# Kernel optimization log

Hardware: AMD Instinct MI355X
Metric: run time of the kernel (lower is better)

The kernel has to match this reference:

```python
import jax, jax.numpy as jnp
import numpy as np

NUM_QUANTIZERS = 8
CODEBOOK_SIZE = 1024
DIM = 256
COMMITMENT_WEIGHT = 0.25


def setup_inputs() -> dict:
    key = jax.random.key(0)
    kz, kc = jax.random.split(key)
    z = jax.random.normal(kz, (32, 1024, DIM), dtype=jnp.float32)
    # nn.init.uniform_(cb.weight, -1/codebook_size, 1/codebook_size) per quantizer
    bound = 1.0 / CODEBOOK_SIZE
    codebooks = jax.random.uniform(
        kc, (NUM_QUANTIZERS, CODEBOOK_SIZE, DIM), dtype=jnp.float32,
        minval=-bound, maxval=bound)
    return {"z": z, "codebooks": codebooks}


def reference(z, codebooks):
    """z: [B,T,D]; codebooks: [Q,K,D]. Returns (quantized, all_indices [Q,B,T], vq_loss)."""
    sg = jax.lax.stop_gradient

    def step(carry, cb):
        residual, quantized = carry
        # squared-distance matrix [B,T,K]: ||r||^2 - 2 r.cb^T + ||cb||^2
        dists = (jnp.sum(residual * residual, axis=-1, keepdims=True)
                 - 2.0 * jnp.einsum('btd,kd->btk', residual, cb)
                 + jnp.sum(cb * cb, axis=-1))
        indices = jnp.argmin(dists, axis=-1)            # [B,T]
        q = cb[indices]                                  # [B,T,D]
        codebook_loss = jnp.mean((q - sg(residual)) ** 2)
        commit_loss = jnp.mean((residual - sg(q)) ** 2)
        loss = codebook_loss + COMMITMENT_WEIGHT * commit_loss
        q_st = residual + sg(q - residual)               # straight-through
        quantized = quantized + q_st
        residual = residual - q_st
        return (residual, quantized), (indices, loss)

    init = (z, jnp.zeros_like(z))
    (_, quantized), (all_indices, losses) = jax.lax.scan(step, init, codebooks)
    vq_loss = jnp.sum(losses)
    return quantized, all_indices, vq_loss
```

## Files before the change

kernel.cpp:

```cpp
#include <hip/hip_runtime.h>

#define QN 8
#define KN 1024
#define DN 256
#define NROWS 32768
#define IDX_BASE 8388608
#define LOSS_OFF 8650752
#define MARGIN 5e-3f
#define LCAP 3072u

#define WS_LOSS 0
#define WS_CNORM 8
#define WS_CSPLIT 12623880

#define SM_RES   0
#define SM_LCAND 66560
#define SM_CHC   78848
#define SM_ANS   79360
#define SM_RMIN  79616
#define SM_LCNT  79872
#define SM_BYTES 79888
#define RESW 260

typedef __attribute__((ext_vector_type(8))) short short8v;
typedef __attribute__((ext_vector_type(4))) float f32x4;

static __device__ __forceinline__ unsigned short f2bf(float x) {
  unsigned int u = __float_as_uint(x);
  unsigned int r = (u + 0x7fffu + ((u >> 16) & 1u)) >> 16;
  return (unsigned short)r;
}

static __device__ __forceinline__ unsigned cvt_pk_bf16(float lo, float hi) {
  unsigned r;
  asm("v_cvt_pk_bf16_f32 %0, %1, %2" : "=v"(r) : "v"(lo), "v"(hi));
  return r;
}

__device__ __forceinline__ float sum256_sq_np(const float* p) {
  float h[2];
#pragma unroll
  for (int half = 0; half < 2; ++half) {
    const float* a = p + half * 128;
    float r[8];
#pragma unroll
    for (int j = 0; j < 8; ++j) r[j] = __fmul_rn(a[j], a[j]);
    for (int i = 8; i < 128; i += 8) {
#pragma unroll
      for (int j = 0; j < 8; ++j) r[j] = __fadd_rn(r[j], __fmul_rn(a[i + j], a[i + j]));
    }
    h[half] = __fadd_rn(__fadd_rn(__fadd_rn(r[0], r[1]), __fadd_rn(r[2], r[3])),
                        __fadd_rn(__fadd_rn(r[4], r[5]), __fadd_rn(r[6], r[7])));
  }
  return __fadd_rn(h[0], h[1]);
}

__global__ void rvq_prep_norm(const float* __restrict__ cb, float* __restrict__ ws) {
  int g = blockIdx.x * blockDim.x + threadIdx.x;
  if (g < 8) ws[WS_LOSS + g] = 0.f;
  if (g < QN * KN) ws[WS_CNORM + g] = sum256_sq_np(cb + (size_t)g * DN);
}

__global__ void rvq_prep_cast(const float* __restrict__ cb, unsigned short* __restrict__ cs) {
  int gid = blockIdx.x * blockDim.x + threadIdx.x;
  uint4* s4 = (uint4*)cs;
#pragma unroll
  for (int k = 0; k < 2; ++k) {
    int ci = gid + k * 131072;
    int q = ci >> 15, rem = ci & 32767;
    int lane = rem & 63, fid = rem >> 6;
    int j = fid & 1, s = (fid >> 1) & 1, kk = (fid >> 2) & 3, wc = (fid >> 4) & 3, c = fid >> 6;
    int code = wc * 32 + j * 16 + (lane & 15);
    int doff = kk * 64 + s * 32 + (lane >> 4) * 8;
    const float4* src = (const float4*)(cb + ((size_t)(q * 1024 + c * 128 + code) * 256 + doff));
    float4 v0 = src[0], v1 = src[1];
    uint4 w;
    w.x = (unsigned)f2bf(v0.x) | ((unsigned)f2bf(v0.y) << 16);
    w.y = (unsigned)f2bf(v0.z) | ((unsigned)f2bf(v0.w) << 16);
    w.z = (unsigned)f2bf(v1.x) | ((unsigned)f2bf(v1.y) << 16);
    w.w = (unsigned)f2bf(v1.z) | ((unsigned)f2bf(v1.w) << 16);
    s4[ci] = w;
  }
}

__global__ __launch_bounds__(256, 2) void rvq_fused_all(const float* __restrict__ z,
                                                        const float* __restrict__ cb,
                                                        float* __restrict__ ws,
                                                        float* __restrict__ out) {
  extern __shared__ __align__(16) char smem[];
  float* RES = (float*)(smem + SM_RES);
  unsigned int* lcand = (unsigned int*)(smem + SM_LCAND);
  unsigned long long* chc = (unsigned long long*)(smem + SM_CHC);
  float* an_s = (float*)(smem + SM_ANS);
  unsigned int* rowmin = (unsigned int*)(smem + SM_RMIN);
  unsigned int* lcnt = (unsigned int*)(smem + SM_LCNT);

  const int tid = threadIdx.x;
  const int row0 = blockIdx.x * 64;
  const int wv = tid >> 6, lane = tid & 63, quad = lane >> 4, l15 = lane & 15;
  const int wr = wv >> 1, wc = wv & 1;

  const float4* zb = (const float4*)(z + (size_t)row0 * DN);
#pragma unroll
  for (int k = 0; k < 16; ++k) {
    int fi = k * 256 + tid;
    int rr = fi >> 6, dd = (fi & 63) * 4;
    *(float4*)&RES[rr * RESW + dd] = zb[fi];
  }
  __syncthreads();
  if (tid < 64) an_s[tid] = sum256_sq_np(&RES[tid * RESW]);

  const uint4* Bf = (const uint4*)((const unsigned short*)(ws + WS_CSPLIT));

#pragma unroll 1
  for (int q = 0; q < QN; ++q) {
    const bool last = (q == QN - 1);

    __syncthreads();
    if (tid < 64) {
      rowmin[tid] = 0x7f7fffffu;
      chc[tid] = ~0ull;
    }
    if (tid == 0) *lcnt = 0u;

    short8v areg[2][2][4];
#pragma unroll
    for (int kk = 0; kk < 4; ++kk) {
#pragma unroll
      for (int s = 0; s < 2; ++s) {
#pragma unroll
        for (int i = 0; i < 2; ++i) {
          int ra = wr * 32 + i * 16 + l15;
          int g = kk * 8 + s * 4 + quad;
          const float* fp = &RES[ra * RESW + g * 8];
          float4 v0 = *(const float4*)fp;
          float4 v1 = *(const float4*)(fp + 4);
          uint4 w;
          w.x = cvt_pk_bf16(v0.x, v0.y);
          w.y = cvt_pk_bf16(v0.z, v0.w);
          w.z = cvt_pk_bf16(v1.x, v1.y);
          w.w = cvt_pk_bf16(v1.z, v1.w);
          areg[i][s][kk] = *(short8v*)&w;
        }
      }
    }
    __syncthreads();

    const uint4* Bl = Bf + ((size_t)q * 32768 + lane);
    const float* cnq_g = ws + WS_CNORM + q * KN;
    for (int c = 0; c < 8; ++c) {
      float cnr[4];
#pragma unroll
      for (int j = 0; j < 4; ++j) cnr[j] = cnq_g[c * 128 + wc * 64 + j * 16 + l15];

      f32x4 acc[2][4];
#pragma unroll
      for (int i = 0; i < 2; ++i)
#pragma unroll
        for (int j = 0; j < 4; ++j) acc[i][j] = (f32x4){0.f, 0.f, 0.f, 0.f};

      const uint4* Bc = Bl + c * 4096;
#pragma unroll
      for (int kk = 0; kk < 4; ++kk) {
        uint4 braw[2][4];
#pragma unroll
        for (int s = 0; s < 2; ++s)
#pragma unroll
          for (int j = 0; j < 4; ++j)
            braw[s][j] = Bc[(wc * 2 + (j >> 1)) * 1024 + kk * 256 + s * 128 + (j & 1) * 64];
#pragma unroll
        for (int s = 0; s < 2; ++s)
#pragma unroll
          for (int i = 0; i < 2; ++i)
#pragma unroll
            for (int j = 0; j < 4; ++j)
              acc[i][j] = __builtin_amdgcn_mfma_f32_16x16x32_bf16(
                  areg[i][s][kk], *(const short8v*)&braw[s][j], acc[i][j], 0, 0, 0);
      }

#pragma unroll
      for (int i = 0; i < 2; ++i) {
#pragma unroll
        for (int reg = 0; reg < 4; ++reg) {
          int rl = wr * 32 + i * 16 + quad * 4 + reg;
          float an = an_s[rl];
          float bd = 3.402823466e+38f;
#pragma unroll
          for (int j = 0; j < 4; ++j) {
            float d = __fadd_rn(__fadd_rn(an, -2.0f * acc[i][j][reg]), cnr[j]);
            bd = (d < bd) ? d : bd;
          }
#pragma unroll
          for (int m = 1; m <= 8; m <<= 1) {
            float od = __shfl_xor(bd, m, 64);
            bd = (od < bd) ? od : bd;
          }
          if (l15 == 0) atomicMin(&rowmin[rl], __float_as_uint(bd));
        }
      }
      __syncthreads();
#pragma unroll
      for (int i = 0; i < 2; ++i) {
#pragma unroll
        for (int reg = 0; reg < 4; ++reg) {
          int rl = wr * 32 + i * 16 + quad * 4 + reg;
          float an = an_s[rl];
          float thr = __uint_as_float(rowmin[rl]) + MARGIN;
#pragma unroll
          for (int j = 0; j < 4; ++j) {
            float d = __fadd_rn(__fadd_rn(an, -2.0f * acc[i][j][reg]), cnr[j]);
            if (d <= thr) {
              unsigned int p = atomicAdd(lcnt, 1u);
              if (p < LCAP)
                lcand[p] = ((unsigned)rl << 10) |
                           (unsigned)(c * 128 + wc * 64 + j * 16 + l15);
            }
          }
        }
      }
    }
    __syncthreads();

    const float* cbq = cb + (size_t)q * KN * DN;
    const float* cnq = ws + WS_CNORM + q * KN;
    unsigned int n = *lcnt;
    if (n <= LCAP) {
      for (unsigned int e = tid; e < n; e += 256u) {
        unsigned int en = lcand[e];
        int rl = en >> 10, code = en & 1023;
        const float* r = &RES[rl * RESW];
        const float* cc = cbq + (size_t)code * DN;
        float B = 0.f;
#pragma unroll 16
        for (int d = 0; d < DN; ++d) B = fmaf(r[d], cc[d], B);
        float de = __fadd_rn(__fadd_rn(an_s[rl], -2.0f * B), cnq[code]);
        unsigned long long key = ((unsigned long long)__float_as_uint(de) << 32) | (unsigned)code;
        atomicMin(&chc[rl], key);
      }
    } else {
      for (int e = tid; e < 64 * 1024; e += 256) {
        int rl = e >> 10, code = e & 1023;
        const float* r = &RES[rl * RESW];
        const float* cc = cbq + (size_t)code * DN;
        float B = 0.f;
#pragma unroll 16
        for (int d = 0; d < DN; ++d) B = fmaf(r[d], cc[d], B);
        float de = __fadd_rn(__fadd_rn(an_s[rl], -2.0f * B), cnq[code]);
        unsigned long long key = ((unsigned long long)__float_as_uint(de) << 32) | (unsigned)code;
        atomicMin(&chc[rl], key);
      }
    }
    __syncthreads();

    const int ur = tid >> 4, ud = tid & 15;
    float lp = 0.f;
    for (int pass = 0; pass < 4; ++pass) {
      int rl = pass * 16 + ur;
      int row = row0 + rl;
      int idx = (int)(chc[rl] & 1023u);
      if (ud == 0) out[IDX_BASE + (size_t)q * NROWS + row] = (float)idx;

      float4* r4 = (float4*)&RES[rl * RESW + ud * 16];
      const float4* q4 = (const float4*)(cb + ((size_t)q * KN + idx) * DN) + ud * 4;
      float4 rnb[4];
#pragma unroll
      for (int t = 0; t < 4; ++t) {
        float4 r = r4[t], qv = q4[t];
        float tx = __fadd_rn(qv.x, -r.x), ty = __fadd_rn(qv.y, -r.y);
        float tz = __fadd_rn(qv.z, -r.z), tw = __fadd_rn(qv.w, -r.w);
        float sx = __fadd_rn(r.x, tx), sy = __fadd_rn(r.y, ty);
        float sz = __fadd_rn(r.z, tz), sw = __fadd_rn(r.w, tw);
        rnb[t] = make_float4(__fadd_rn(r.x, -sx), __fadd_rn(r.y, -sy),
                             __fadd_rn(r.z, -sz), __fadd_rn(r.w, -sw));
        lp = fmaf(tx, tx, lp); lp = fmaf(ty, ty, lp);
        lp = fmaf(tz, tz, lp); lp = fmaf(tw, tw, lp);
      }

      if (last) {
        const float4* z4 = (const float4*)(z + (size_t)row * DN) + ud * 4;
        float4* o4 = (float4*)(out + (size_t)row * DN) + ud * 4;
#pragma unroll
        for (int t = 0; t < 4; ++t) {
          float4 zv = z4[t];
          o4[t] = make_float4(__fadd_rn(zv.x, -rnb[t].x), __fadd_rn(zv.y, -rnb[t].y),
                              __fadd_rn(zv.z, -rnb[t].z), __fadd_rn(zv.w, -rnb[t].w));
        }
      } else {
#pragma unroll
        for (int t = 0; t < 4; ++t) r4[t] = rnb[t];
      }
    }

#pragma unroll
    for (int off = 32; off > 0; off >>= 1) lp += __shfl_down(lp, off, 64);
    if (lane == 0) atomicAdd(ws + WS_LOSS + q, lp);

    if (!last) {
      __syncthreads();
      if (tid < 64) an_s[tid] = sum256_sq_np(&RES[tid * RESW]);
    }
  }
}

__global__ void rvq_fin(const float* __restrict__ ws, float* __restrict__ out) {
  if (blockIdx.x == 0 && threadIdx.x == 0) {
    float vq = 0.f;
    for (int q = 0; q < QN; ++q) {
      float m = ws[WS_LOSS + q] / 8388608.0f;
      float l = __fadd_rn(m, 0.25f * m);
      vq = __fadd_rn(vq, l);
    }
    out[LOSS_OFF] = vq;
  }
}

extern "C" void kernel_launch(void* const* d_in, const int* in_sizes, int n_in,
                              void* d_out, int out_size, void* d_ws, size_t ws_size,
                              hipStream_t stream) {
  const float* z = (const float*)d_in[0];
  const float* cb = (const float*)d_in[1];
  float* out = (float*)d_out;
  float* ws = (float*)d_ws;

  hipLaunchKernelGGL(rvq_prep_norm, dim3(32), dim3(256), 0, stream, cb, ws);
  hipLaunchKernelGGL(rvq_prep_cast, dim3(512), dim3(256), 0, stream, cb,
                     (unsigned short*)(ws + WS_CSPLIT));
  hipLaunchKernelGGL(rvq_fused_all, dim3(512), dim3(256), SM_BYTES, stream, z, cb, ws, out);
  hipLaunchKernelGGL(rvq_fin, dim3(1), dim3(64), 0, stream, ws, out);
}
```

Baseline: 794.1 us.

## Split codebook tiles across eight waves and drop the threshold barrier

Doubles the block to 512 threads, so each wave scores 32 codes per chunk instead of 64, which halves the per-wave accumulators and B loads. The barrier between the row-minimum reduction and candidate filtering is removed: each wave filters against the lower of its own minimum and whatever shared minimum is already visible. That threshold is looser, so more candidates can be emitted and the LCAP brute-force fallback becomes more likely. Loss is accumulated in shared memory and written with one global atomic per block per quantizer. The new launch bounds (512, 4) cap registers tightly even though the A fragments alone are large, which risks register spills.

```diff
diff --git a/kernel.cpp b/kernel.cpp
--- a/kernel.cpp
+++ b/kernel.cpp
@@ -83,7 +83,7 @@
   }
 }
 
-__global__ __launch_bounds__(256, 2) void rvq_fused_all(const float* __restrict__ z,
+__global__ __launch_bounds__(512, 4) void rvq_fused_all(const float* __restrict__ z,
                                                         const float* __restrict__ cb,
                                                         float* __restrict__ ws,
                                                         float* __restrict__ out) {
@@ -94,19 +94,21 @@
   float* an_s = (float*)(smem + SM_ANS);
   unsigned int* rowmin = (unsigned int*)(smem + SM_RMIN);
   unsigned int* lcnt = (unsigned int*)(smem + SM_LCNT);
+  float* lsum = (float*)(smem + SM_LCNT + 4);
 
   const int tid = threadIdx.x;
   const int row0 = blockIdx.x * 64;
   const int wv = tid >> 6, lane = tid & 63, quad = lane >> 4, l15 = lane & 15;
-  const int wr = wv >> 1, wc = wv & 1;
+  const int wr = wv >> 2, wc = wv & 3;
 
   const float4* zb = (const float4*)(z + (size_t)row0 * DN);
 #pragma unroll
-  for (int k = 0; k < 16; ++k) {
-    int fi = k * 256 + tid;
+  for (int k = 0; k < 8; ++k) {
+    int fi = k * 512 + tid;
     int rr = fi >> 6, dd = (fi & 63) * 4;
     *(float4*)&RES[rr * RESW + dd] = zb[fi];
   }
+  if (tid == 0) *lsum = 0.f;
   __syncthreads();
   if (tid < 64) an_s[tid] = sum256_sq_np(&RES[tid * RESW]);
 
@@ -146,34 +148,34 @@
     }
     __syncthreads();
 
-    const uint4* Bl = Bf + ((size_t)q * 32768 + lane);
+    const uint4* Bl = Bf + ((size_t)q * 32768 + wc * 1024 + lane);
     const float* cnq_g = ws + WS_CNORM + q * KN;
     for (int c = 0; c < 8; ++c) {
-      float cnr[4];
-#pragma unroll
-      for (int j = 0; j < 4; ++j) cnr[j] = cnq_g[c * 128 + wc * 64 + j * 16 + l15];
-
-      f32x4 acc[2][4];
+      float cnr[2];
+#pragma unroll
+      for (int j = 0; j < 2; ++j) cnr[j] = cnq_g[c * 128 + wc * 32 + j * 16 + l15];
+
+      f32x4 acc[2][2];
 #pragma unroll
       for (int i = 0; i < 2; ++i)
 #pragma unroll
-        for (int j = 0; j < 4; ++j) acc[i][j] = (f32x4){0.f, 0.f, 0.f, 0.f};
+        for (int j = 0; j < 2; ++j) acc[i][j] = (f32x4){0.f, 0.f, 0.f, 0.f};
 
       const uint4* Bc = Bl + c * 4096;
 #pragma unroll
       for (int kk = 0; kk < 4; ++kk) {
-        uint4 braw[2][4];
+        uint4 braw[2][2];
 #pragma unroll
         for (int s = 0; s < 2; ++s)
 #pragma unroll
-          for (int j = 0; j < 4; ++j)
-            braw[s][j] = Bc[(wc * 2 + (j >> 1)) * 1024 + kk * 256 + s * 128 + (j & 1) * 64];
+          for (int j = 0; j < 2; ++j)
+            braw[s][j] = Bc[kk * 256 + s * 128 + j * 64];
 #pragma unroll
         for (int s = 0; s < 2; ++s)
 #pragma unroll
           for (int i = 0; i < 2; ++i)
 #pragma unroll
-            for (int j = 0; j < 4; ++j)
+            for (int j = 0; j < 2; ++j)
               acc[i][j] = __builtin_amdgcn_mfma_f32_16x16x32_bf16(
                   areg[i][s][kk], *(const short8v*)&braw[s][j], acc[i][j], 0, 0, 0);
       }
@@ -184,37 +186,29 @@
         for (int reg = 0; reg < 4; ++reg) {
           int rl = wr * 32 + i * 16 + quad * 4 + reg;
           float an = an_s[rl];
+          float d0 = __fadd_rn(__fadd_rn(an, -2.0f * acc[i][0][reg]), cnr[0]);
+          float d1 = __fadd_rn(__fadd_rn(an, -2.0f * acc[i][1][reg]), cnr[1]);
           float bd = 3.402823466e+38f;
-#pragma unroll
-          for (int j = 0; j < 4; ++j) {
-            float d = __fadd_rn(__fadd_rn(an, -2.0f * acc[i][j][reg]), cnr[j]);
-            bd = (d < bd) ? d : bd;
-          }
+          bd = (d0 < bd) ? d0 : bd;
+          bd = (d1 < bd) ? d1 : bd;
 #pragma unroll
           for (int m = 1; m <= 8; m <<= 1) {
             float od = __shfl_xor(bd, m, 64);
             bd = (od < bd) ? od : bd;
           }
+          float rmf = __uint_as_float(rowmin[rl]);
           if (l15 == 0) atomicMin(&rowmin[rl], __float_as_uint(bd));
-        }
-      }
-      __syncthreads();
-#pragma unroll
-      for (int i = 0; i < 2; ++i) {
-#pragma unroll
-        for (int reg = 0; reg < 4; ++reg) {
-          int rl = wr * 32 + i * 16 + quad * 4 + reg;
-          float an = an_s[rl];
-          float thr = __uint_as_float(rowmin[rl]) + MARGIN;
-#pragma unroll
-          for (int j = 0; j < 4; ++j) {
-            float d = __fadd_rn(__fadd_rn(an, -2.0f * acc[i][j][reg]), cnr[j]);
-            if (d <= thr) {
-              unsigned int p = atomicAdd(lcnt, 1u);
-              if (p < LCAP)
-                lcand[p] = ((unsigned)rl << 10) |
-                           (unsigned)(c * 128 + wc * 64 + j * 16 + l15);
-            }
+          float tb = (bd < rmf) ? bd : rmf;
+          float thr = tb + MARGIN;
+          if (d0 <= thr) {
+            unsigned int p = atomicAdd(lcnt, 1u);
+            if (p < LCAP)
+              lcand[p] = ((unsigned)rl << 10) | (unsigned)(c * 128 + wc * 32 + l15);
+          }
+          if (d1 <= thr) {
+            unsigned int p = atomicAdd(lcnt, 1u);
+            if (p < LCAP)
+              lcand[p] = ((unsigned)rl << 10) | (unsigned)(c * 128 + wc * 32 + 16 + l15);
           }
         }
       }
@@ -225,7 +219,7 @@
     const float* cnq = ws + WS_CNORM + q * KN;
     unsigned int n = *lcnt;
     if (n <= LCAP) {
-      for (unsigned int e = tid; e < n; e += 256u) {
+      for (unsigned int e = tid; e < n; e += 512u) {
         unsigned int en = lcand[e];
         int rl = en >> 10, code = en & 1023;
         const float* r = &RES[rl * RESW];
@@ -238,7 +232,7 @@
         atomicMin(&chc[rl], key);
       }
     } else {
-      for (int e = tid; e < 64 * 1024; e += 256) {
+      for (int e = tid; e < 64 * 1024; e += 512) {
         int rl = e >> 10, code = e & 1023;
         const float* r = &RES[rl * RESW];
         const float* cc = cbq + (size_t)code * DN;
@@ -254,8 +248,8 @@
 
     const int ur = tid >> 4, ud = tid & 15;
     float lp = 0.f;
-    for (int pass = 0; pass < 4; ++pass) {
-      int rl = pass * 16 + ur;
+    for (int pass = 0; pass < 2; ++pass) {
+      int rl = pass * 32 + ur;
       int row = row0 + rl;
       int idx = (int)(chc[rl] & 1023u);
       if (ud == 0) out[IDX_BASE + (size_t)q * NROWS + row] = (float)idx;
@@ -293,11 +287,13 @@
 
 #pragma unroll
     for (int off = 32; off > 0; off >>= 1) lp += __shfl_down(lp, off, 64);
-    if (lane == 0) atomicAdd(ws + WS_LOSS + q, lp);
-
-    if (!last) {
-      __syncthreads();
-      if (tid < 64) an_s[tid] = sum256_sq_np(&RES[tid * RESW]);
+    if (lane == 0) atomicAdd(lsum, lp);
+
+    __syncthreads();
+    if (!last && tid < 64) an_s[tid] = sum256_sq_np(&RES[tid * RESW]);
+    if (tid == 0) {
+      atomicAdd(ws + WS_LOSS + q, *lsum);
+      *lsum = 0.f;
     }
   }
 }
@@ -325,6 +321,6 @@
   hipLaunchKernelGGL(rvq_prep_norm, dim3(32), dim3(256), 0, stream, cb, ws);
   hipLaunchKernelGGL(rvq_prep_cast, dim3(512), dim3(256), 0, stream, cb,
                      (unsigned short*)(ws + WS_CSPLIT));
-  hipLaunchKernelGGL(rvq_fused_all, dim3(512), dim3(256), SM_BYTES, stream, z, cb, ws, out);
+  hipLaunchKernelGGL(rvq_fused_all, dim3(512), dim3(512), SM_BYTES, stream, z, cb, ws, out);
   hipLaunchKernelGGL(rvq_fin, dim3(1), dim3(64), 0, stream, ws, out);
 }
```

Measured after the change: 719.1 us. 9.4% less time.
